# Kernel optimization log

Measured on AMD Instinct MI355X. Metric: run time of the kernel, lower is better.

## Reference

```python
import jax, jax.numpy as jnp
import numpy as np

B, D, F, P = 65536, 256, 512, 256


def setup_inputs() -> dict:
    key = jax.random.key(0)
    k_x, k_f, k_p, k_a, k_b, k_t = jax.random.split(key, 6)
    x = jax.random.normal(k_x, (B, D), dtype=jnp.float32)
    # reset_parameters: uniform(-0.27, 1)
    features = jax.random.uniform(k_f, (F, D), dtype=jnp.float32, minval=-0.27, maxval=1.0)
    prototypes = jax.random.uniform(k_p, (P, D), dtype=jnp.float32, minval=-0.27, maxval=1.0)
    # alpha/beta/theta init to zeros in the module; use small random values so the
    # output is non-trivial for kernel correctness checking.
    alpha = jax.random.normal(k_a, (1,), dtype=jnp.float32) * 0.1
    beta = jax.random.normal(k_b, (1,), dtype=jnp.float32) * 0.1
    theta = jax.random.normal(k_t, (1,), dtype=jnp.float32) * 0.1
    return {"x": x, "features": features, "prototypes": prototypes,
            "alpha": alpha, "beta": beta, "theta": theta}


def reference(x, features, prototypes, alpha, beta, theta):
    # Shared projections
    x_features = x @ features.T                 # [B, F]
    p_features = prototypes @ features.T        # [P, F]
    x_present = jax.nn.relu(x_features)         # [B, F]
    p_present = jax.nn.relu(p_features)         # [P, F]
    x_weighted = x_features * x_present         # [B, F]
    p_weighted = p_features * p_present         # [P, F]

    # Tversky terms
    common = x_weighted @ p_weighted.T                          # [B, P]
    x_weighted_sum = jnp.sum(x_weighted, axis=1, keepdims=True)  # [B, 1]
    x_p_interaction = x_weighted @ p_present.T                  # [B, P]
    x_distinctive = x_weighted_sum - x_p_interaction            # [B, P]
    p_weighted_sum = jnp.sum(p_weighted, axis=1)[None, :]        # [1, P]
    x_p_weighted_interaction = x_present @ p_weighted.T         # [B, P]
    p_distinctive = p_weighted_sum - x_p_weighted_interaction   # [B, P]

    return theta * common - alpha * x_distinctive - beta * p_distinctive
```

## Files before the change

### kernel.cpp

```cpp
#include <hip/hip_runtime.h>
#include <cstdint>
#include <cstddef>

#define Bsz 65536
#define Dsz 256
#define Fsz 512
#define Psz 256

typedef __attribute__((ext_vector_type(8))) short short8;
typedef __attribute__((ext_vector_type(4))) short short4v;
typedef __attribute__((ext_vector_type(4))) float float4v;
typedef __attribute__((ext_vector_type(16))) float float16v;
typedef __attribute__((ext_vector_type(4))) unsigned uint4v;

__device__ inline short f2bf(float f) {
    unsigned u = __builtin_bit_cast(unsigned, f);
    u = (u + 0x7FFFu + ((u >> 16) & 1u)) >> 16;
    return (short)u;
}
__device__ inline float bf2f(short s) {
    unsigned u = ((unsigned)(unsigned short)s) << 16;
    return __builtin_bit_cast(float, u);
}
__device__ inline unsigned cvt_pk_bf16(float lo, float hi) {
    unsigned r;
    asm("v_cvt_pk_bf16_f32 %0, %1, %2" : "=v"(r) : "v"(lo), "v"(hi));
    return r;
}
__device__ inline void gl_lds16(const short* g, short* lds) {
    __builtin_amdgcn_global_load_lds((const __attribute__((address_space(1))) unsigned*)g,
                                     (__attribute__((address_space(3))) unsigned*)lds,
                                     16, 0, 0);
}


#define SBPITCH 136

__global__ __launch_bounds__(256, 2) void k_pre(
    const float* __restrict__ prototypes, const float* __restrict__ features,
    const float* __restrict__ alpha_p, const float* __restrict__ beta_p,
    const float* __restrict__ theta_p,
    short* __restrict__ featbB, short* __restrict__ pab, float* __restrict__ pws_part)
{
    __shared__ char lds[65536 + 17408];
    short* FB = (short*)lds;
    short* As = (short*)(lds + 65536);
    short* Sb = (short*)(lds + 65536);

    const int t = threadIdx.x;
    const int w = t >> 6, lane = t & 63, l15 = lane & 15, l4 = lane >> 4;
    const int rowg = blockIdx.x >> 2, nc = blockIdx.x & 3;
    const float alpha = *alpha_p, beta = *beta_p, theta = *theta_p;

    #pragma unroll
    for (int it = 0; it < 16; ++it) {
        int u = it * 256 + t;
        int ftl = u >> 10, dtl = (u >> 6) & 15, ln = u & 63;
        const float* src = features + (size_t)(nc * 128 + ftl * 32 + (ln & 31)) * Dsz
                         + dtl * 16 + (ln >> 5) * 8;
        float4v v0 = *(const float4v*)src;
        float4v v1 = *(const float4v*)(src + 4);
        uint4v uv;
        uv.x = cvt_pk_bf16(v0.x, v0.y);
        uv.y = cvt_pk_bf16(v0.z, v0.w);
        uv.z = cvt_pk_bf16(v1.x, v1.y);
        uv.w = cvt_pk_bf16(v1.z, v1.w);
        short8 sv = __builtin_bit_cast(short8, uv);
        *(short8*)&FB[u * 8] = sv;
        if (rowg == 0) {
            int go = (((nc * 4 + ftl) * 16 + dtl) * 64 + ln) * 8;
            *(short8*)&featbB[go] = sv;
        }
    }

    float4v acc[2][4];
    #pragma unroll
    for (int a = 0; a < 2; ++a)
        #pragma unroll
        for (int b = 0; b < 4; ++b) acc[a][b] = (float4v){0.f, 0.f, 0.f, 0.f};

    const float* pbase = prototypes + (size_t)rowg * 64 * Dsz;

    for (int kc = 0; kc < 4; ++kc) {
        __syncthreads();
        #pragma unroll
        for (int j = 0; j < 4; ++j) {
            int idx = j * 1024 + t * 4;
            int r = idx >> 6, c = idx & 63;
            float4v v = *(const float4v*)(pbase + (size_t)r * Dsz + kc * 64 + c);
            int unit = r * 8 + ((c >> 3) ^ (r & 7));
            short4v s4; s4.x = f2bf(v.x); s4.y = f2bf(v.y); s4.z = f2bf(v.z); s4.w = f2bf(v.w);
            *(short4v*)((char*)As + unit * 16 + (c & 7) * 2) = s4;
        }
        __syncthreads();
        #pragma unroll
        for (int kk = 0; kk < 2; ++kk) {
            short8 af[2], bfr[4];
            const int k8 = kk * 4 + l4;
            #pragma unroll
            for (int tm = 0; tm < 2; ++tm) {
                int m = (w & 1) * 32 + tm * 16 + l15;
                af[tm] = *(const short8*)&As[(m * 8 + (k8 ^ (m & 7))) * 8];
            }
            #pragma unroll
            for (int tn = 0; tn < 4; ++tn) {
                int fl = ((w >> 1) * 4 + tn) * 16 + l15;
                int dtl = kc * 4 + kk * 2 + (l4 >> 1);
                int lnp = (fl & 31) + 32 * (l4 & 1);
                bfr[tn] = *(const short8*)&FB[(((fl >> 5) * 16 + dtl) * 64 + lnp) * 8];
            }
            #pragma unroll
            for (int tm = 0; tm < 2; ++tm)
                #pragma unroll
                for (int tn = 0; tn < 4; ++tn)
                    acc[tm][tn] = __builtin_amdgcn_mfma_f32_16x16x32_bf16(af[tm], bfr[tn], acc[tm][tn], 0, 0, 0);
        }
    }
    __syncthreads();
    #pragma unroll
    for (int tm = 0; tm < 2; ++tm)
        #pragma unroll
        for (int tn = 0; tn < 4; ++tn)
            #pragma unroll
            for (int r = 0; r < 4; ++r) {
                int row = (w & 1) * 32 + tm * 16 + l4 * 4 + r;
                int col = (w >> 1) * 64 + tn * 16 + l15;
                Sb[row * SBPITCH + col] = f2bf(acc[tm][tn][r]);
            }
    __syncthreads();
    #pragma unroll
    for (int rep = 0; rep < 4; ++rep) {
        int u = rep * 256 + t;
        int row = u >> 4, i = u & 15;
        short8 sv = *(const short8*)&Sb[row * SBPITCH + i * 8];
        uint4v u0, u1;
        float sum = 0.f;
        #pragma unroll
        for (int e = 0; e < 8; ++e) {
            float pf = bf2f(sv[e]);
            float pp = fmaxf(pf, 0.f);
            float pw = pf * pp;
            float a0 = theta * pw + alpha * (pp - 1.f);
            float b0 = beta * pw;
            sum += pw;
            unsigned pk = cvt_pk_bf16(a0, b0);
            if (e < 4) u0[e] = pk; else u1[e - 4] = pk;
        }
        int p = rowg * 64 + row;
        int c = 4 * nc + (i >> 2), s2 = i & 3, pt = p >> 5;
        int base = ((c * 4 + s2) * 8 + pt) * 512;
        *(short8*)&pab[base + (p & 31) * 8] = __builtin_bit_cast(short8, u0);
        *(short8*)&pab[base + ((p & 31) + 32) * 8] = __builtin_bit_cast(short8, u1);
        #pragma unroll
        for (int mk = 1; mk < 16; mk <<= 1) sum += __shfl_xor(sum, mk, 64);
        if (l15 == 0) pws_part[nc * 256 + p] = -beta * sum;
    }
}

__global__ __launch_bounds__(512, 2) void k_main(
    const float* __restrict__ x, const short* __restrict__ featbB,
    const short* __restrict__ pab, const float* __restrict__ pws_part,
    float* __restrict__ out)
{
    __shared__ short FBL[2][8192];
    __shared__ short PBL[2][16384];

    const int t = threadIdx.x;
    const int w = t >> 6, lane = t & 63, l31 = lane & 31, h = lane >> 5;
    const int mt = w & 3, pth4 = (w >> 2) * 4;
    const size_t row0 = (size_t)blockIdx.x * 128;
    const int lane8 = lane * 8;

    {
        const short* fsrc = featbB + lane8;
        gl_lds16(fsrc + (2 * w) * 512,     &FBL[0][(2 * w) * 512]);
        gl_lds16(fsrc + (2 * w + 1) * 512, &FBL[0][(2 * w + 1) * 512]);
        const short* psrc = pab + lane8;
        #pragma unroll
        for (int i = 0; i < 4; ++i)
            gl_lds16(psrc + (4 * w + i) * 512, &PBL[0][(4 * w + i) * 512]);
    }
    __builtin_amdgcn_sched_barrier(0);

    short8 xf[16];
    {
        const float* xr = x + (row0 + mt * 32 + l31) * Dsz + h * 8;
        #pragma unroll
        for (int dt = 0; dt < 16; ++dt) {
            float4v v0 = *(const float4v*)(xr + dt * 16);
            float4v v1 = *(const float4v*)(xr + dt * 16 + 4);
            uint4v uv;
            uv.x = cvt_pk_bf16(v0.x, v0.y);
            uv.y = cvt_pk_bf16(v0.z, v0.w);
            uv.z = cvt_pk_bf16(v1.x, v1.y);
            uv.w = cvt_pk_bf16(v1.z, v1.w);
            xf[dt] = __builtin_bit_cast(short8, uv);
        }
    }

    float16v acc[4];
    #pragma unroll
    for (int a = 0; a < 4; ++a)
        #pragma unroll
        for (int e = 0; e < 16; ++e) acc[a][e] = 0.f;

    #pragma unroll 1
    for (int c = 0; c < 16; ++c) {
        const int cur = c & 1, nxt = cur ^ 1;
        const int cn = (c + 1) & 15;

        __syncthreads();

        {
            const short* fsrc = featbB + cn * 8192 + lane8;
            gl_lds16(fsrc + (2 * w) * 512,     &FBL[nxt][(2 * w) * 512]);
            gl_lds16(fsrc + (2 * w + 1) * 512, &FBL[nxt][(2 * w + 1) * 512]);
            const short* psrc = pab + (size_t)cn * 16384 + lane8;
            #pragma unroll
            for (int i = 0; i < 4; ++i)
                gl_lds16(psrc + (4 * w + i) * 512, &PBL[nxt][(4 * w + i) * 512]);
        }
        __builtin_amdgcn_sched_barrier(0);

        float16v C1a, C1b;
        #pragma unroll
        for (int e = 0; e < 16; ++e) { C1a[e] = 0.f; C1b[e] = 0.f; }
        short8 PBr[8];
        #pragma unroll
        for (int g = 0; g < 4; ++g) {
            short8 fbf[4];
            #pragma unroll
            for (int i = 0; i < 4; ++i)
                fbf[i] = *(const short8*)&FBL[cur][(g * 4 + i) * 512 + lane8];
            if (g == 2) {
                #pragma unroll
                for (int k = 0; k < 8; ++k)
                    PBr[k] = *(const short8*)&PBL[cur][(((k >> 2)) * 8 + pth4 + (k & 3)) * 512 + lane8];
            }
            __builtin_amdgcn_s_setprio(1);
            #pragma unroll
            for (int i = 0; i < 4; ++i) {
                if (((g * 4 + i) & 1) == 0)
                    C1a = __builtin_amdgcn_mfma_f32_32x32x16_bf16(fbf[i], xf[g * 4 + i], C1a, 0, 0, 0);
                else
                    C1b = __builtin_amdgcn_mfma_f32_32x32x16_bf16(fbf[i], xf[g * 4 + i], C1b, 0, 0, 0);
            }
            __builtin_amdgcn_s_setprio(0);
        }
        float16v C1;
        #pragma unroll
        for (int e = 0; e < 16; ++e) C1[e] = C1a[e] + C1b[e];

        #pragma unroll
        for (int s = 0; s < 4; ++s) {
            if (s == 2) {
                #pragma unroll
                for (int k = 0; k < 8; ++k)
                    PBr[k] = *(const short8*)&PBL[cur][((2 + (k >> 2)) * 8 + pth4 + (k & 3)) * 512 + lane8];
            }
            uint4v uf;
            #pragma unroll
            for (int q = 0; q < 4; ++q) {
                float xv = C1[4 * s + q];
                float xp = fmaxf(xv, 0.f);
                uf[q] = cvt_pk_bf16(xv * xp, xp);
            }
            short8 A2f = __builtin_bit_cast(short8, uf);
            __builtin_amdgcn_s_setprio(1);
            #pragma unroll
            for (int ptl = 0; ptl < 4; ++ptl)
                acc[ptl] = __builtin_amdgcn_mfma_f32_32x32x16_bf16(A2f, PBr[(s & 1) * 4 + ptl], acc[ptl], 0, 0, 0);
            __builtin_amdgcn_s_setprio(0);
        }
    }

    #pragma unroll
    for (int ptl = 0; ptl < 4; ++ptl) {
        int pcol = (pth4 + ptl) * 32 + l31;
        float pn = pws_part[pcol] + pws_part[256 + pcol] + pws_part[512 + pcol] + pws_part[768 + pcol];
        #pragma unroll
        for (int r = 0; r < 16; ++r) {
            size_t m = row0 + mt * 32 + (r & 3) + 8 * (r >> 2) + 4 * h;
            out[m * Psz + pcol] = acc[ptl][r] + pn;
        }
    }
}

extern "C" void kernel_launch(void* const* d_in, const int* in_sizes, int n_in,
                              void* d_out, int out_size, void* d_ws, size_t ws_size,
                              hipStream_t stream) {
    const float* x          = (const float*)d_in[0];
    const float* features   = (const float*)d_in[1];
    const float* prototypes = (const float*)d_in[2];
    const float* alpha      = (const float*)d_in[3];
    const float* beta       = (const float*)d_in[4];
    const float* theta      = (const float*)d_in[5];
    float* out = (float*)d_out;

    char* ws = (char*)d_ws;
    short* featbB   = (short*)(ws);
    short* pab      = (short*)(ws + 262144);
    float* pws_part = (float*)(ws + 786432);

    hipLaunchKernelGGL(k_pre,  dim3(16),  dim3(256), 0, stream,
                       prototypes, features, alpha, beta, theta, featbB, pab, pws_part);
    hipLaunchKernelGGL(k_main, dim3(512), dim3(512), 0, stream,
                       x, featbB, pab, pws_part, out);
}
```

Before: 198.4 us.

## Software-pipeline GEMM1 of next chunk with GEMM2 of previous chunk

Restructures the main loop so the second-stage MFMAs for chunk c-1 are interleaved with the first-stage MFMAs for chunk c, instead of running the two stages back to back. This breaks the dependency stall where GEMM2 waits on the C1 accumulation and the relu/bf16 conversion. The prototype tile buffer grows to triple buffering (extra 32KB LDS) so the previous chunk's data stays resident, which may reduce occupancy from two blocks per CU and adds register pressure.

Result: no change. 200.9 us (+1.3%).

```diff
diff --git a/kernel.cpp b/kernel.cpp
--- a/kernel.cpp
+++ b/kernel.cpp
@@ -162,8 +162,8 @@
     const short* __restrict__ pab, const float* __restrict__ pws_part,
     float* __restrict__ out)
 {
-    __shared__ short FBL[2][8192];
-    __shared__ short PBL[2][16384];
+    __shared__ short FBL[2 * 8192];
+    __shared__ short PBL[3 * 16384];
 
     const int t = threadIdx.x;
     const int w = t >> 6, lane = t & 63, l31 = lane & 31, h = lane >> 5;
@@ -171,15 +171,17 @@
     const size_t row0 = (size_t)blockIdx.x * 128;
     const int lane8 = lane * 8;
 
-    {
-        const short* fsrc = featbB + lane8;
-        gl_lds16(fsrc + (2 * w) * 512,     &FBL[0][(2 * w) * 512]);
-        gl_lds16(fsrc + (2 * w + 1) * 512, &FBL[0][(2 * w + 1) * 512]);
-        const short* psrc = pab + lane8;
+    auto stage = [&](int cn, int foff, int poff) {
+        const short* fsrc = featbB + cn * 8192 + lane8;
+        gl_lds16(fsrc + (2 * w) * 512,     &FBL[foff + (2 * w) * 512]);
+        gl_lds16(fsrc + (2 * w + 1) * 512, &FBL[foff + (2 * w + 1) * 512]);
+        const short* psrc = pab + cn * 16384 + lane8;
         #pragma unroll
         for (int i = 0; i < 4; ++i)
-            gl_lds16(psrc + (4 * w + i) * 512, &PBL[0][(4 * w + i) * 512]);
-    }
+            gl_lds16(psrc + (4 * w + i) * 512, &PBL[poff + (4 * w + i) * 512]);
+    };
+
+    stage(0, 0, 0);
     __builtin_amdgcn_sched_barrier(0);
 
     short8 xf[16];
@@ -204,64 +206,61 @@
         #pragma unroll
         for (int e = 0; e < 16; ++e) acc[a][e] = 0.f;
 
-    #pragma unroll 1
-    for (int c = 0; c < 16; ++c) {
-        const int cur = c & 1, nxt = cur ^ 1;
-        const int cn = (c + 1) & 15;
-
-        __syncthreads();
-
-        {
-            const short* fsrc = featbB + cn * 8192 + lane8;
-            gl_lds16(fsrc + (2 * w) * 512,     &FBL[nxt][(2 * w) * 512]);
-            gl_lds16(fsrc + (2 * w + 1) * 512, &FBL[nxt][(2 * w + 1) * 512]);
-            const short* psrc = pab + (size_t)cn * 16384 + lane8;
-            #pragma unroll
-            for (int i = 0; i < 4; ++i)
-                gl_lds16(psrc + (4 * w + i) * 512, &PBL[nxt][(4 * w + i) * 512]);
-        }
-        __builtin_amdgcn_sched_barrier(0);
-
-        float16v C1a, C1b;
-        #pragma unroll
-        for (int e = 0; e < 16; ++e) { C1a[e] = 0.f; C1b[e] = 0.f; }
-        short8 PBr[8];
+    __syncthreads();
+    stage(1, 8192, 16384);
+    __builtin_amdgcn_sched_barrier(0);
+
+    float16v C1p;
+    {
+        float16v Ca, Cb;
+        #pragma unroll
+        for (int e = 0; e < 16; ++e) { Ca[e] = 0.f; Cb[e] = 0.f; }
         #pragma unroll
         for (int g = 0; g < 4; ++g) {
             short8 fbf[4];
             #pragma unroll
             for (int i = 0; i < 4; ++i)
-                fbf[i] = *(const short8*)&FBL[cur][(g * 4 + i) * 512 + lane8];
-            if (g == 2) {
-                #pragma unroll
-                for (int k = 0; k < 8; ++k)
-                    PBr[k] = *(const short8*)&PBL[cur][(((k >> 2)) * 8 + pth4 + (k & 3)) * 512 + lane8];
-            }
+                fbf[i] = *(const short8*)&FBL[(g * 4 + i) * 512 + lane8];
             __builtin_amdgcn_s_setprio(1);
             #pragma unroll
             for (int i = 0; i < 4; ++i) {
-                if (((g * 4 + i) & 1) == 0)
-                    C1a = __builtin_amdgcn_mfma_f32_32x32x16_bf16(fbf[i], xf[g * 4 + i], C1a, 0, 0, 0);
-                else
-                    C1b = __builtin_amdgcn_mfma_f32_32x32x16_bf16(fbf[i], xf[g * 4 + i], C1b, 0, 0, 0);
+                if (i & 1) Cb = __builtin_amdgcn_mfma_f32_32x32x16_bf16(fbf[i], xf[g * 4 + i], Cb, 0, 0, 0);
+                else       Ca = __builtin_amdgcn_mfma_f32_32x32x16_bf16(fbf[i], xf[g * 4 + i], Ca, 0, 0, 0);
             }
             __builtin_amdgcn_s_setprio(0);
         }
-        float16v C1;
-        #pragma unroll
-        for (int e = 0; e < 16; ++e) C1[e] = C1a[e] + C1b[e];
-
-        #pragma unroll
-        for (int s = 0; s < 4; ++s) {
-            if (s == 2) {
-                #pragma unroll
-                for (int k = 0; k < 8; ++k)
-                    PBr[k] = *(const short8*)&PBL[cur][((2 + (k >> 2)) * 8 + pth4 + (k & 3)) * 512 + lane8];
-            }
+        #pragma unroll
+        for (int e = 0; e < 16; ++e) C1p[e] = Ca[e] + Cb[e];
+    }
+
+    int pb_prev = 0, pb_cur = 16384, pb_nxt = 32768;
+    #pragma unroll 1
+    for (int c = 1; c < 16; ++c) {
+        const int fcur = (c & 1) * 8192;
+
+        __syncthreads();
+
+        if (c < 15) stage(c + 1, fcur ^ 8192, pb_nxt);
+        __builtin_amdgcn_sched_barrier(0);
+
+        float16v Ca, Cb;
+        #pragma unroll
+        for (int e = 0; e < 16; ++e) { Ca[e] = 0.f; Cb[e] = 0.f; }
+
+        #pragma unroll
+        for (int g = 0; g < 4; ++g) {
+            short8 fbf[4];
+            #pragma unroll
+            for (int i = 0; i < 4; ++i)
+                fbf[i] = *(const short8*)&FBL[fcur + (g * 4 + i) * 512 + lane8];
+            short8 PBr[4];
+            #pragma unroll
+            for (int ptl = 0; ptl < 4; ++ptl)
+                PBr[ptl] = *(const short8*)&PBL[pb_prev + (g * 8 + pth4 + ptl) * 512 + lane8];
             uint4v uf;
             #pragma unroll
             for (int q = 0; q < 4; ++q) {
-                float xv = C1[4 * s + q];
+                float xv = C1p[4 * g + q];
                 float xp = fmaxf(xv, 0.f);
                 uf[q] = cvt_pk_bf16(xv * xp, xp);
             }
@@ -269,9 +268,37 @@
             __builtin_amdgcn_s_setprio(1);
             #pragma unroll
             for (int ptl = 0; ptl < 4; ++ptl)
-                acc[ptl] = __builtin_amdgcn_mfma_f32_32x32x16_bf16(A2f, PBr[(s & 1) * 4 + ptl], acc[ptl], 0, 0, 0);
+                acc[ptl] = __builtin_amdgcn_mfma_f32_32x32x16_bf16(A2f, PBr[ptl], acc[ptl], 0, 0, 0);
+            #pragma unroll
+            for (int i = 0; i < 4; ++i) {
+                if (i & 1) Cb = __builtin_amdgcn_mfma_f32_32x32x16_bf16(fbf[i], xf[g * 4 + i], Cb, 0, 0, 0);
+                else       Ca = __builtin_amdgcn_mfma_f32_32x32x16_bf16(fbf[i], xf[g * 4 + i], Ca, 0, 0, 0);
+            }
             __builtin_amdgcn_s_setprio(0);
         }
+        #pragma unroll
+        for (int e = 0; e < 16; ++e) C1p[e] = Ca[e] + Cb[e];
+
+        int tmp = pb_prev; pb_prev = pb_cur; pb_cur = pb_nxt; pb_nxt = tmp;
+    }
+
+    #pragma unroll
+    for (int s = 0; s < 4; ++s) {
+        short8 PBr[4];
+        #pragma unroll
+        for (int ptl = 0; ptl < 4; ++ptl)
+            PBr[ptl] = *(const short8*)&PBL[pb_prev + (s * 8 + pth4 + ptl) * 512 + lane8];
+        uint4v uf;
+        #pragma unroll
+        for (int q = 0; q < 4; ++q) {
+            float xv = C1p[4 * s + q];
+            float xp = fmaxf(xv, 0.f);
+            uf[q] = cvt_pk_bf16(xv * xp, xp);
+        }
+        short8 A2f = __builtin_bit_cast(short8, uf);
+        #pragma unroll
+        for (int ptl = 0; ptl < 4; ++ptl)
+            acc[ptl] = __builtin_amdgcn_mfma_f32_32x32x16_bf16(A2f, PBr[ptl], acc[ptl], 0, 0, 0);
     }
 
     #pragma unroll
```

## Halve block tile to 64 rows with 256 threads and single-buffered PAB LDS

Applied to the files above, without the earlier changes.

The main kernel now uses 256-thread blocks covering 64 rows each, launched as 1024 blocks, instead of 512-thread blocks covering 128 rows. The prototype/PAB staging buffer drops from double to single buffering, with an extra barrier per chunk, while the features buffer stays double-buffered. PAB fragments are now loaded per sub-step rather than prefetched into eight registers. The goal is lower LDS use and more resident blocks per CU, which could improve occupancy and latency hiding. The cost is that each features/PAB chunk is reused across fewer rows, so the kernel moves more global-to-LDS traffic and hits more barriers, and the PAB load is no longer overlapped with the first GEMM.

New measurement: 188.8 us. 4.8% less time.

```diff
diff --git a/kernel.cpp b/kernel.cpp
--- a/kernel.cpp
+++ b/kernel.cpp
@@ -157,29 +157,35 @@
     }
 }
 
-__global__ __launch_bounds__(512, 2) void k_main(
+__global__ __launch_bounds__(256, 2) void k_main(
     const float* __restrict__ x, const short* __restrict__ featbB,
     const short* __restrict__ pab, const float* __restrict__ pws_part,
     float* __restrict__ out)
 {
     __shared__ short FBL[2][8192];
-    __shared__ short PBL[2][16384];
+    __shared__ short PBL[16384];
 
     const int t = threadIdx.x;
     const int w = t >> 6, lane = t & 63, l31 = lane & 31, h = lane >> 5;
-    const int mt = w & 3, pth4 = (w >> 2) * 4;
-    const size_t row0 = (size_t)blockIdx.x * 128;
+    const int mt = w & 1, pth = w >> 1;
+    const size_t row0 = (size_t)blockIdx.x * 64;
     const int lane8 = lane * 8;
 
-    {
-        const short* fsrc = featbB + lane8;
-        gl_lds16(fsrc + (2 * w) * 512,     &FBL[0][(2 * w) * 512]);
-        gl_lds16(fsrc + (2 * w + 1) * 512, &FBL[0][(2 * w + 1) * 512]);
-        const short* psrc = pab + lane8;
+    auto stage_fb = [&](int cn, int buf) {
+        const short* src = featbB + cn * 8192 + lane8;
         #pragma unroll
         for (int i = 0; i < 4; ++i)
-            gl_lds16(psrc + (4 * w + i) * 512, &PBL[0][(4 * w + i) * 512]);
-    }
+            gl_lds16(src + (4 * w + i) * 512, &FBL[buf][(4 * w + i) * 512]);
+    };
+    auto stage_pab = [&](int cn) {
+        const short* src = pab + (size_t)cn * 16384 + lane8;
+        #pragma unroll
+        for (int i = 0; i < 8; ++i)
+            gl_lds16(src + (8 * w + i) * 512, &PBL[(8 * w + i) * 512]);
+    };
+
+    stage_fb(0, 0);
+    stage_pab(0);
     __builtin_amdgcn_sched_barrier(0);
 
     short8 xf[16];
@@ -204,60 +210,48 @@
         #pragma unroll
         for (int e = 0; e < 16; ++e) acc[a][e] = 0.f;
 
+    __syncthreads();
+
     #pragma unroll 1
     for (int c = 0; c < 16; ++c) {
-        const int cur = c & 1, nxt = cur ^ 1;
-        const int cn = (c + 1) & 15;
-
-        __syncthreads();
-
-        {
-            const short* fsrc = featbB + cn * 8192 + lane8;
-            gl_lds16(fsrc + (2 * w) * 512,     &FBL[nxt][(2 * w) * 512]);
-            gl_lds16(fsrc + (2 * w + 1) * 512, &FBL[nxt][(2 * w + 1) * 512]);
-            const short* psrc = pab + (size_t)cn * 16384 + lane8;
-            #pragma unroll
-            for (int i = 0; i < 4; ++i)
-                gl_lds16(psrc + (4 * w + i) * 512, &PBL[nxt][(4 * w + i) * 512]);
-        }
+        const int cur = c & 1;
+
+        if (c) {
+            __syncthreads();
+            stage_pab(c);
+        }
+        if (c < 15) stage_fb(c + 1, cur ^ 1);
         __builtin_amdgcn_sched_barrier(0);
 
-        float16v C1a, C1b;
-        #pragma unroll
-        for (int e = 0; e < 16; ++e) { C1a[e] = 0.f; C1b[e] = 0.f; }
-        short8 PBr[8];
+        float16v Ca, Cb;
+        #pragma unroll
+        for (int e = 0; e < 16; ++e) { Ca[e] = 0.f; Cb[e] = 0.f; }
         #pragma unroll
         for (int g = 0; g < 4; ++g) {
             short8 fbf[4];
             #pragma unroll
             for (int i = 0; i < 4; ++i)
                 fbf[i] = *(const short8*)&FBL[cur][(g * 4 + i) * 512 + lane8];
-            if (g == 2) {
-                #pragma unroll
-                for (int k = 0; k < 8; ++k)
-                    PBr[k] = *(const short8*)&PBL[cur][(((k >> 2)) * 8 + pth4 + (k & 3)) * 512 + lane8];
-            }
             __builtin_amdgcn_s_setprio(1);
             #pragma unroll
             for (int i = 0; i < 4; ++i) {
-                if (((g * 4 + i) & 1) == 0)
-                    C1a = __builtin_amdgcn_mfma_f32_32x32x16_bf16(fbf[i], xf[g * 4 + i], C1a, 0, 0, 0);
-                else
-                    C1b = __builtin_amdgcn_mfma_f32_32x32x16_bf16(fbf[i], xf[g * 4 + i], C1b, 0, 0, 0);
+                if (i & 1) Cb = __builtin_amdgcn_mfma_f32_32x32x16_bf16(fbf[i], xf[g * 4 + i], Cb, 0, 0, 0);
+                else       Ca = __builtin_amdgcn_mfma_f32_32x32x16_bf16(fbf[i], xf[g * 4 + i], Ca, 0, 0, 0);
             }
             __builtin_amdgcn_s_setprio(0);
         }
         float16v C1;
         #pragma unroll
-        for (int e = 0; e < 16; ++e) C1[e] = C1a[e] + C1b[e];
+        for (int e = 0; e < 16; ++e) C1[e] = Ca[e] + Cb[e];
+
+        __syncthreads();
 
         #pragma unroll
         for (int s = 0; s < 4; ++s) {
-            if (s == 2) {
-                #pragma unroll
-                for (int k = 0; k < 8; ++k)
-                    PBr[k] = *(const short8*)&PBL[cur][((2 + (k >> 2)) * 8 + pth4 + (k & 3)) * 512 + lane8];
-            }
+            short8 PBr[4];
+            #pragma unroll
+            for (int ptl = 0; ptl < 4; ++ptl)
+                PBr[ptl] = *(const short8*)&PBL[(s * 8 + pth * 4 + ptl) * 512 + lane8];
             uint4v uf;
             #pragma unroll
             for (int q = 0; q < 4; ++q) {
@@ -269,14 +263,14 @@
             __builtin_amdgcn_s_setprio(1);
             #pragma unroll
             for (int ptl = 0; ptl < 4; ++ptl)
-                acc[ptl] = __builtin_amdgcn_mfma_f32_32x32x16_bf16(A2f, PBr[(s & 1) * 4 + ptl], acc[ptl], 0, 0, 0);
+                acc[ptl] = __builtin_amdgcn_mfma_f32_32x32x16_bf16(A2f, PBr[ptl], acc[ptl], 0, 0, 0);
             __builtin_amdgcn_s_setprio(0);
         }
     }
 
     #pragma unroll
     for (int ptl = 0; ptl < 4; ++ptl) {
-        int pcol = (pth4 + ptl) * 32 + l31;
+        int pcol = (pth * 4 + ptl) * 32 + l31;
         float pn = pws_part[pcol] + pws_part[256 + pcol] + pws_part[512 + pcol] + pws_part[768 + pcol];
         #pragma unroll
         for (int r = 0; r < 16; ++r) {
@@ -302,8 +296,8 @@
     short* pab      = (short*)(ws + 262144);
     float* pws_part = (float*)(ws + 786432);
 
-    hipLaunchKernelGGL(k_pre,  dim3(16),  dim3(256), 0, stream,
+    hipLaunchKernelGGL(k_pre,  dim3(16),   dim3(256), 0, stream,
                        prototypes, features, alpha, beta, theta, featbB, pab, pws_part);
-    hipLaunchKernelGGL(k_main, dim3(512), dim3(512), 0, stream,
+    hipLaunchKernelGGL(k_main, dim3(1024), dim3(256), 0, stream,
                        x, featbB, pab, pws_part, out);
 }
```
